# Kernel optimization log

Hardware: AMD Instinct MI355X
Metric: run time of the kernel (lower is better)

Reference implementation:

```python
import jax, jax.numpy as jnp
import numpy as np

B, T, D, U = 64, 512, 1024, 1024


def hard_sigmoid(x):
    # keras hard_sigmoid: clip(0.2*x + 0.5, 0, 1)
    return jnp.clip(0.2 * x + 0.5, 0.0, 1.0)


def setup_inputs() -> dict:
    key = jax.random.key(0)
    ks = jax.random.split(key, 6)
    x = jax.random.normal(ks[0], (B, T, D), jnp.float32)
    # glorot-ish scaled params
    kernel = jax.random.normal(ks[1], (D, 4 * U), jnp.float32) * (1.0 / np.sqrt(D).astype(np.float32))
    recurrent_kernel = jax.random.normal(ks[2], (U, 4 * U), jnp.float32) * (1.0 / np.sqrt(U).astype(np.float32))
    peephole_kernel = jax.random.normal(ks[3], (U, 3 * U), jnp.float32) * (1.0 / np.sqrt(U).astype(np.float32))
    projection_kernel = jax.random.normal(ks[4], (U, U), jnp.float32) * (1.0 / np.sqrt(U).astype(np.float32))
    # unit_forget_bias: [zeros(U), ones(U), zeros(2U)] for (i, f, c, o)
    bias = jnp.concatenate([jnp.zeros((U,), jnp.float32), jnp.ones((U,), jnp.float32), jnp.zeros((2 * U,), jnp.float32)])
    h0 = jnp.zeros((B, U), jnp.float32)
    c0 = jnp.zeros((B, U), jnp.float32)
    return {"x": x, "h0": h0, "c0": c0, "kernel": kernel, "recurrent_kernel": recurrent_kernel,
            "peephole_kernel": peephole_kernel, "projection_kernel": projection_kernel, "bias": bias}


def reference(x, h0, c0, kernel, recurrent_kernel, peephole_kernel, projection_kernel, bias):
    U_ = h0.shape[-1]
    Pi = peephole_kernel[:, :U_]
    Pf = peephole_kernel[:, U_:2 * U_]
    Po = peephole_kernel[:, 2 * U_:3 * U_]

    def step(carry, x_t):
        h, c = carry
        # fused gate pre-activations: [B, 4U]
        z = x_t @ kernel + h @ recurrent_kernel + bias
        zi, zf, zc, zo = jnp.split(z, 4, axis=-1)
        i = hard_sigmoid(zi + c @ Pi)            # input gate w/ peephole on c_{t-1}
        f = hard_sigmoid(zf + c @ Pf)            # forget gate w/ peephole on c_{t-1}
        c_new = f * c + i * jnp.tanh(zc)
        o = hard_sigmoid(zo + c_new @ Po)        # output gate w/ peephole on c_t
        # residual LSTM: project tanh(c_t), add residual input, gate by o
        h_new = o * (jnp.tanh(c_new) @ projection_kernel + x_t)
        return (h_new, c_new), h_new

    xs = jnp.swapaxes(x, 0, 1)  # [T, B, D]
    (_, _), hs = jax.lax.scan(step, (h0, c0), xs)
    return jnp.swapaxes(hs, 0, 1)  # [B, T, U]
```

## Files before the change

kernel.cpp:

```cpp
#include <hip/hip_runtime.h>
#include <cstdint>
#include <cstddef>

#define NB 64
#define NT 512
#define ND 1024
#define NU 1024

typedef short s16x8 __attribute__((ext_vector_type(8)));
typedef float f32x4 __attribute__((ext_vector_type(4)));
typedef unsigned short u16;

__device__ __forceinline__ u16 f2bf(float f) {
  unsigned int u = __float_as_uint(f);
  u += 0x7fffu + ((u >> 16) & 1u);
  return (u16)(u >> 16);
}
__device__ __forceinline__ float bf2f(u16 s) {
  return __uint_as_float(((unsigned int)s) << 16);
}
__device__ __forceinline__ float hsig(float x) {
  return fminf(fmaxf(0.2f * x + 0.5f, 0.0f), 1.0f);
}
__device__ __forceinline__ f32x4 mfma16(s16x8 a, s16x8 b, f32x4 c) {
  return __builtin_amdgcn_mfma_f32_16x16x32_bf16(a, b, c, 0, 0, 0);
}

__device__ __forceinline__ void atomic_swap_u32(unsigned int* p, unsigned int v) {
  asm volatile("global_atomic_swap %0, %1, off" :: "v"(p), "v"(v) : "memory");
}

#define WAIT_VM0() do { \
    asm volatile("s_waitcnt vmcnt(0)" ::: "memory"); \
    __builtin_amdgcn_sched_barrier(0); \
  } while (0)

__global__ __launch_bounds__(256) void xw_gemm(const float* __restrict__ X,
                                               const float* __restrict__ W,
                                               u16* __restrict__ XW) {
  __shared__ u16 Al[128][72];
  __shared__ u16 Bl[128][72];
  const int tid = threadIdx.x;
  const int lane = tid & 63;
  const int wv = tid >> 6;
  const int m0 = (blockIdx.x >> 5) * 128;
  const int n0 = (blockIdx.x & 31) * 128;
  f32x4 acc[4][4];
#pragma unroll
  for (int i = 0; i < 4; ++i)
#pragma unroll
    for (int j = 0; j < 4; ++j) acc[i][j] = (f32x4){0.f, 0.f, 0.f, 0.f};

  for (int kt = 0; kt < 1024; kt += 64) {
    {
      const int r = tid >> 1, hh = (tid & 1) * 32;
      const float* src = X + (size_t)(m0 + r) * 1024 + kt + hh;
      u16* dst = &Al[r][hh];
#pragma unroll
      for (int j = 0; j < 8; ++j) {
        float4 v = ((const float4*)src)[j];
        dst[j * 4 + 0] = f2bf(v.x); dst[j * 4 + 1] = f2bf(v.y);
        dst[j * 4 + 2] = f2bf(v.z); dst[j * 4 + 3] = f2bf(v.w);
      }
    }
    {
      const int kr = tid >> 2, q = (tid & 3) * 32;
      const float* src = W + (size_t)(kt + kr) * 4096 + n0 + q;
#pragma unroll
      for (int j = 0; j < 8; ++j) {
        float4 v = ((const float4*)src)[j];
        const int n = q + j * 4;
        Bl[n + 0][kr] = f2bf(v.x); Bl[n + 1][kr] = f2bf(v.y);
        Bl[n + 2][kr] = f2bf(v.z); Bl[n + 3][kr] = f2bf(v.w);
      }
    }
    __syncthreads();
    const int wm = (wv >> 1) * 64, wn = (wv & 1) * 64;
    const int row = lane & 15, kq = (lane >> 4) * 8;
#pragma unroll
    for (int ks = 0; ks < 2; ++ks) {
      s16x8 af[4], bq[4];
#pragma unroll
      for (int i = 0; i < 4; ++i) af[i] = *(const s16x8*)&Al[wm + i * 16 + row][ks * 32 + kq];
#pragma unroll
      for (int j = 0; j < 4; ++j) bq[j] = *(const s16x8*)&Bl[wn + j * 16 + row][ks * 32 + kq];
#pragma unroll
      for (int i = 0; i < 4; ++i)
#pragma unroll
        for (int j = 0; j < 4; ++j) acc[i][j] = mfma16(af[i], bq[j], acc[i][j]);
    }
    __syncthreads();
  }
  const int wm = (wv >> 1) * 64, wn = (wv & 1) * 64;
  const int col16 = lane & 15, rq = (lane >> 4) * 4;
#pragma unroll
  for (int i = 0; i < 4; ++i)
#pragma unroll
    for (int j = 0; j < 4; ++j)
#pragma unroll
      for (int q = 0; q < 4; ++q) {
        const int m = m0 + wm + i * 16 + rq + q;
        const int n = n0 + wn + j * 16 + col16;
        const int t = m & 511, b = m >> 9;
        const int g = n >> 10, uu = n & 1023;
        const int ugrp = uu >> 3, ul2 = uu & 7;
        XW[(((size_t)ugrp * 512 + t) * 64 + b) * 32 + g * 8 + ul2] = f2bf(acc[i][j][q]);
      }
}

__global__ void init_comm(const float* __restrict__ h0, const float* __restrict__ c0,
                          u16* hbuf, u16* cbuf) {
  const int i = blockIdx.x * 256 + threadIdx.x;
  hbuf[i] = f2bf(h0[i]);
  cbuf[i] = f2bf(c0[i]);
}

__device__ __forceinline__ void gbar(unsigned int* flags, int bid, int tid, unsigned int ep) {
  __syncthreads();
  if (tid == 0) atomic_swap_u32(flags + bid * 16, ep);
  unsigned int* f = flags + tid * 16;
  for (;;) {
    unsigned int v;
    asm volatile("global_load_dword %0, %1, off sc0 sc1\n\ts_waitcnt vmcnt(0)"
                 : "=v"(v) : "v"(f) : "memory");
    if (v >= ep) break;
    __builtin_amdgcn_s_sleep(1);
  }
  __syncthreads();
}

#define WLDS_B   (64 * 1032 * 2)
#define ZOFF     WLDS_B
#define POFF     (ZOFF + 32 * 33 * 4)
#define OOFF     (POFF + 32 * 17 * 4)
#define SMEM_B   (OOFF + 32 * 17 * 4)

__global__ __launch_bounds__(256, 1) void lstm_loop(
    const float* __restrict__ rec, const float* __restrict__ peep,
    const float* __restrict__ projw, const float* __restrict__ bias,
    const float* __restrict__ x, const u16* __restrict__ xw,
    float* __restrict__ out,
    u16* hbuf, u16* cbuf, u16* thbuf,
    unsigned int* flags, const float* __restrict__ c0) {
  extern __shared__ char smem[];
  u16 (*wlds)[1032] = (u16(*)[1032])smem;
  float (*zlds)[33] = (float(*)[33])(smem + ZOFF);
  float (*plds)[17] = (float(*)[17])(smem + POFF);
  float (*olds)[17] = (float(*)[17])(smem + OOFF);

  const int tid = threadIdx.x;
  const int lane = tid & 63;
  const int wv = tid >> 6;
  const int bid = blockIdx.x;
  const int ugrp = bid >> 1;
  const int row0 = (bid & 1) * 32;
  const int u0 = ugrp * 8;

  for (int g = 0; g < 8; ++g) {
    const int c = g * 8 + (tid & 3) * 2;
    const float* sp; int stride, scol;
    if (c < 32)      { sp = rec;   stride = 4096; scol = (c >> 3) * 1024 + u0 + (c & 7); }
    else if (c < 48) { sp = peep;  stride = 3072; scol = ((c - 32) >> 3) * 1024 + u0 + (c & 7); }
    else if (c < 56) { sp = peep;  stride = 3072; scol = 2048 + u0 + (c & 7); }
    else             { sp = projw; stride = 1024; scol = u0 + (c - 56); }
#pragma unroll 4
    for (int p = 0; p < 16; ++p) {
      const int k = p * 64 + (tid >> 2);
      float2 v = *(const float2*)(sp + (size_t)k * stride + scol);
      wlds[c][k] = f2bf(v.x);
      wlds[c + 1][k] = f2bf(v.y);
    }
  }

  const int r = tid >> 3;
  const int ul = tid & 7;
  const int brow = row0 + r;
  const int u = u0 + ul;
  const float b_i = bias[u], b_f = bias[1024 + u], b_c = bias[2048 + u], b_o = bias[3072 + u];
  float cst = c0[brow * 1024 + u];

  const int fcol = lane & 15;
  const int kofs = (lane >> 4) * 8;

  s16x8 av[32];
  if (wv < 2) {
    const u16* ap = cbuf + (size_t)(row0 + wv * 16 + fcol) * 1024 + kofs;
#pragma unroll
    for (int kt = 0; kt < 32; ++kt)
      asm volatile("global_load_dwordx4 %0, %1, off sc0 sc1"
                   : "=v"(av[kt]) : "v"(ap + kt * 32));
  }
  WAIT_VM0();
  __syncthreads();

  for (int t = 0; t < NT; ++t) {
    float zo_reg;

    const u16* xr = xw + (((size_t)ugrp * 512 + t) * 64 + brow) * 32;
    const float xw_i = bf2f(xr[ul]);
    const float xw_f = bf2f(xr[8 + ul]);
    const float xw_c = bf2f(xr[16 + ul]);
    const float xw_o = bf2f(xr[24 + ul]);
    const size_t xo = (size_t)brow * (512 * 1024) + (size_t)t * 1024 + u;
    const float xres = x[xo];

    if (wv >= 2) {
      const int rt = wv - 2;
      const u16* ap = hbuf + (size_t)(row0 + rt * 16 + fcol) * 1024 + kofs;
#pragma unroll
      for (int kt = 0; kt < 32; ++kt)
        asm volatile("global_load_dwordx4 %0, %1, off sc0 sc1"
                     : "=v"(av[kt]) : "v"(ap + kt * 32));
      WAIT_VM0();
      f32x4 accA = {0.f, 0.f, 0.f, 0.f}, accB = {0.f, 0.f, 0.f, 0.f};
      const u16* bp0 = &wlds[fcol][kofs];
      const u16* bp1 = &wlds[16 + fcol][kofs];
#pragma unroll
      for (int kt = 0; kt < 32; ++kt) {
        accA = mfma16(av[kt], *(const s16x8*)(bp0 + kt * 32), accA);
        accB = mfma16(av[kt], *(const s16x8*)(bp1 + kt * 32), accB);
      }
      const int srow = rt * 16 + (lane >> 4) * 4;
#pragma unroll
      for (int q = 0; q < 4; ++q) {
        zlds[srow + q][fcol] = accA[q];
        zlds[srow + q][16 + fcol] = accB[q];
      }
    } else {
      f32x4 accP = {0.f, 0.f, 0.f, 0.f};
      const u16* bp = &wlds[32 + fcol][kofs];
#pragma unroll
      for (int kt = 0; kt < 32; ++kt)
        accP = mfma16(av[kt], *(const s16x8*)(bp + kt * 32), accP);
      const int srow = wv * 16 + (lane >> 4) * 4;
#pragma unroll
      for (int q = 0; q < 4; ++q) plds[srow + q][fcol] = accP[q];
    }
    __syncthreads();
    {
      const float zi = zlds[r][ul]      + xw_i + b_i + plds[r][ul];
      const float zf = zlds[r][8 + ul]  + xw_f + b_f + plds[r][8 + ul];
      const float zc = zlds[r][16 + ul] + xw_c + b_c;
      zo_reg         = zlds[r][24 + ul] + xw_o + b_o;
      const float ig = hsig(zi), fg = hsig(zf);
      cst = fg * cst + ig * tanhf(zc);
      const float th = tanhf(cst);
      const unsigned int cb = f2bf(cst), tb = f2bf(th);
      const unsigned int cpart = (unsigned int)__shfl_xor((int)cb, 1);
      const unsigned int tpart = (unsigned int)__shfl_xor((int)tb, 1);
      if ((ul & 1) == 0) {
        atomic_swap_u32((unsigned int*)(cbuf + brow * 1024 + u), (cpart << 16) | cb);
        atomic_swap_u32((unsigned int*)(thbuf + brow * 1024 + u), (tpart << 16) | tb);
      }
    }
    WAIT_VM0();
    gbar(flags, bid, tid, 2 * t + 1);

    {
      const int prt = wv & 1;
      const u16* ap = ((wv < 2) ? (const u16*)cbuf : (const u16*)thbuf)
                      + (size_t)(row0 + prt * 16 + fcol) * 1024 + kofs;
#pragma unroll
      for (int kt = 0; kt < 32; ++kt)
        asm volatile("global_load_dwordx4 %0, %1, off sc0 sc1"
                     : "=v"(av[kt]) : "v"(ap + kt * 32));
      WAIT_VM0();
      f32x4 acc = {0.f, 0.f, 0.f, 0.f};
      const u16* bp = &wlds[48 + fcol][kofs];
#pragma unroll
      for (int kt = 0; kt < 32; ++kt)
        acc = mfma16(av[kt], *(const s16x8*)(bp + kt * 32), acc);
      const int srow = prt * 16 + (lane >> 4) * 4;
      if (wv < 2) {
        if (fcol < 8) {
#pragma unroll
          for (int q = 0; q < 4; ++q) olds[srow + q][fcol] = acc[q];
        }
      } else {
        if (fcol >= 8) {
#pragma unroll
          for (int q = 0; q < 4; ++q) olds[srow + q][fcol] = acc[q];
        }
      }
    }
    __syncthreads();
    {
      const float og = hsig(zo_reg + olds[r][ul]);
      const float pv = olds[r][8 + ul] + xres;
      const float hv = og * pv;
      out[xo] = hv;
      const unsigned int hb = f2bf(hv);
      const unsigned int hpart = (unsigned int)__shfl_xor((int)hb, 1);
      if ((ul & 1) == 0)
        atomic_swap_u32((unsigned int*)(hbuf + brow * 1024 + u), (hpart << 16) | hb);
    }
    WAIT_VM0();
    gbar(flags, bid, tid, 2 * t + 2);
  }
}

extern "C" void kernel_launch(void* const* d_in, const int* in_sizes, int n_in,
                              void* d_out, int out_size, void* d_ws, size_t ws_size,
                              hipStream_t stream) {
  const float* x    = (const float*)d_in[0];
  const float* h0   = (const float*)d_in[1];
  const float* c0   = (const float*)d_in[2];
  const float* W    = (const float*)d_in[3];
  const float* R    = (const float*)d_in[4];
  const float* P    = (const float*)d_in[5];
  const float* PRJ  = (const float*)d_in[6];
  const float* bias = (const float*)d_in[7];
  float* out = (float*)d_out;
  char* ws = (char*)d_ws;

  const size_t XW_BYTES = (size_t)32768 * 4096 * 2;
  size_t off = XW_BYTES;
  u16* xw   = (u16*)ws;
  u16* hbuf = (u16*)(ws + off); off += 131072;
  u16* cbuf = (u16*)(ws + off); off += 131072;
  u16* thb  = (u16*)(ws + off); off += 131072;
  unsigned int* flags = (unsigned int*)(ws + off); off += 16384;
  if (ws_size < off) return;

  (void)hipFuncSetAttribute(reinterpret_cast<const void*>(&lstm_loop),
                            hipFuncAttributeMaxDynamicSharedMemorySize, 160 * 1024);

  hipMemsetAsync(flags, 0, 16384, stream);
  hipLaunchKernelGGL(init_comm, dim3(256), dim3(256), 0, stream, h0, c0, hbuf, cbuf);
  hipLaunchKernelGGL(xw_gemm, dim3(8192), dim3(256), 0, stream, x, W, xw);

  void* args[12];
  args[0] = (void*)&R;    args[1] = (void*)&P;     args[2] = (void*)&PRJ;
  args[3] = (void*)&bias; args[4] = (void*)&x;     args[5] = (void*)&xw;
  args[6] = (void*)&out;  args[7] = (void*)&hbuf;  args[8] = (void*)&cbuf;
  args[9] = (void*)&thb;  args[10] = (void*)&flags; args[11] = (void*)&c0;

  hipError_t e = hipLaunchCooperativeKernel((const void*)lstm_loop, dim3(256), dim3(256),
                                            args, (unsigned int)SMEM_B, stream);
  if (e != hipSuccess) {
    hipLaunchKernelGGL(lstm_loop, dim3(256), dim3(256), SMEM_B, stream,
                       R, P, PRJ, bias, x, xw, out, hbuf, cbuf, thb, flags, c0);
  }
}
```

Baseline: 8.018 ms.

## Prefetch next-step input projections, pack gate layout, and split barrier by batch half

Changes the XW layout so each unit's four gate pre-activations are contiguous, which allows a single dwordx2 load. The next step's XW and residual x values are prefetched into registers during the projection phase, so they overlap the matrix loads instead of stalling the step. The output store moves after the grid barrier, keeping it off the critical path. The barrier now polls only the blocks that share the same batch-row half, which relies on batch rows being independent. That last part depends on how the hidden block mapping is set up, and it adds register pressure and a manual waitcnt ordering.

New measurement: 7.836 ms. -2.3%, faster.

```diff
diff --git a/kernel.cpp b/kernel.cpp
--- a/kernel.cpp
+++ b/kernel.cpp
@@ -9,6 +9,7 @@
 
 typedef short s16x8 __attribute__((ext_vector_type(8)));
 typedef float f32x4 __attribute__((ext_vector_type(4)));
+typedef unsigned int u32x2 __attribute__((ext_vector_type(2)));
 typedef unsigned short u16;
 
 __device__ __forceinline__ u16 f2bf(float f) {
@@ -104,7 +105,7 @@
         const int t = m & 511, b = m >> 9;
         const int g = n >> 10, uu = n & 1023;
         const int ugrp = uu >> 3, ul2 = uu & 7;
-        XW[(((size_t)ugrp * 512 + t) * 64 + b) * 32 + g * 8 + ul2] = f2bf(acc[i][j][q]);
+        XW[(((size_t)ugrp * 512 + t) * 64 + b) * 32 + ul2 * 4 + g] = f2bf(acc[i][j][q]);
       }
 }
 
@@ -118,7 +119,7 @@
 __device__ __forceinline__ void gbar(unsigned int* flags, int bid, int tid, unsigned int ep) {
   __syncthreads();
   if (tid == 0) atomic_swap_u32(flags + bid * 16, ep);
-  unsigned int* f = flags + tid * 16;
+  unsigned int* f = flags + ((((tid & 127) << 1) | (bid & 1)) * 16);
   for (;;) {
     unsigned int v;
     asm volatile("global_load_dword %0, %1, off sc0 sc1\n\ts_waitcnt vmcnt(0)"
@@ -183,6 +184,15 @@
   const int kofs = (lane >> 4) * 8;
 
   s16x8 av[32];
+  u32x2 xwp;
+  float xp;
+
+  {
+    const u16* xr0 = xw + (((size_t)ugrp * 512 + 0) * 64 + brow) * 32 + ul * 4;
+    asm volatile("global_load_dwordx2 %0, %1, off" : "=v"(xwp) : "v"(xr0));
+    const float* xs0 = x + (size_t)brow * (512 * 1024) + u;
+    asm volatile("global_load_dword %0, %1, off" : "=v"(xp) : "v"(xs0));
+  }
   if (wv < 2) {
     const u16* ap = cbuf + (size_t)(row0 + wv * 16 + fcol) * 1024 + kofs;
 #pragma unroll
@@ -194,15 +204,8 @@
   __syncthreads();
 
   for (int t = 0; t < NT; ++t) {
-    float zo_reg;
-
-    const u16* xr = xw + (((size_t)ugrp * 512 + t) * 64 + brow) * 32;
-    const float xw_i = bf2f(xr[ul]);
-    const float xw_f = bf2f(xr[8 + ul]);
-    const float xw_c = bf2f(xr[16 + ul]);
-    const float xw_o = bf2f(xr[24 + ul]);
+    float zo_reg, xres, hv;
     const size_t xo = (size_t)brow * (512 * 1024) + (size_t)t * 1024 + u;
-    const float xres = x[xo];
 
     if (wv >= 2) {
       const int rt = wv - 2;
@@ -238,6 +241,11 @@
     }
     __syncthreads();
     {
+      const float xw_i = bf2f((u16)(xwp[0] & 0xffffu));
+      const float xw_f = bf2f((u16)(xwp[0] >> 16));
+      const float xw_c = bf2f((u16)(xwp[1] & 0xffffu));
+      const float xw_o = bf2f((u16)(xwp[1] >> 16));
+      xres = xp;
       const float zi = zlds[r][ul]      + xw_i + b_i + plds[r][ul];
       const float zf = zlds[r][8 + ul]  + xw_f + b_f + plds[r][8 + ul];
       const float zc = zlds[r][16 + ul] + xw_c + b_c;
@@ -264,7 +272,15 @@
       for (int kt = 0; kt < 32; ++kt)
         asm volatile("global_load_dwordx4 %0, %1, off sc0 sc1"
                      : "=v"(av[kt]) : "v"(ap + kt * 32));
-      WAIT_VM0();
+      {
+        const int tn = (t + 1 < NT) ? (t + 1) : t;
+        const u16* xrn = xw + (((size_t)ugrp * 512 + tn) * 64 + brow) * 32 + ul * 4;
+        asm volatile("global_load_dwordx2 %0, %1, off" : "=v"(xwp) : "v"(xrn));
+        const float* xsn = x + (size_t)brow * (512 * 1024) + (size_t)tn * 1024 + u;
+        asm volatile("global_load_dword %0, %1, off" : "=v"(xp) : "v"(xsn));
+      }
+      asm volatile("s_waitcnt vmcnt(2)" ::: "memory");
+      __builtin_amdgcn_sched_barrier(0);
       f32x4 acc = {0.f, 0.f, 0.f, 0.f};
       const u16* bp = &wlds[48 + fcol][kofs];
 #pragma unroll
@@ -287,8 +303,7 @@
     {
       const float og = hsig(zo_reg + olds[r][ul]);
       const float pv = olds[r][8 + ul] + xres;
-      const float hv = og * pv;
-      out[xo] = hv;
+      hv = og * pv;
       const unsigned int hb = f2bf(hv);
       const unsigned int hpart = (unsigned int)__shfl_xor((int)hb, 1);
       if ((ul & 1) == 0)
@@ -296,6 +311,7 @@
     }
     WAIT_VM0();
     gbar(flags, bid, tid, 2 * t + 2);
+    asm volatile("global_store_dword %0, %1, off" :: "v"(out + xo), "v"(hv) : "memory");
   }
 }
 
```
